# Performance work log

Hardware: AMD Instinct MI355X
Metric: run time of the kernel (lower is better)

## Reference

```python
import jax, jax.numpy as jnp
import numpy as np

N_ENT = 2000
GAT_EMB = 64
GAT_HID = 3
HIDDEN = 256
BATCH = 8
ALPHA = 0.2  # LeakyReLU negative slope
MASK_FILL = jnp.float32(9e-15)  # original fills masked-out logits with 9e-15 (NOT -inf)


def setup_inputs() -> dict:
    key = jax.random.key(0)
    k1, k2, k3, k4, k5, k6 = jax.random.split(key, 6)
    emb = jax.random.normal(k1, (N_ENT, GAT_EMB), dtype=jnp.float32)
    W = jax.random.normal(k2, (GAT_EMB, GAT_HID), dtype=jnp.float32) * 0.2
    a = jax.random.normal(k3, (2 * GAT_HID, 1), dtype=jnp.float32) * 0.2
    fc1_w = jax.random.normal(k4, (HIDDEN, N_ENT * GAT_HID), dtype=jnp.float32) * 0.02
    fc1_b = jax.random.normal(k5, (HIDDEN,), dtype=jnp.float32) * 0.02
    adj = jax.random.randint(k6, (BATCH, N_ENT, N_ENT), 0, 2, dtype=jnp.int32)
    return {"emb": emb, "W": W, "a": a, "fc1_w": fc1_w, "fc1_b": fc1_b, "adj": adj}


def reference(emb, W, a, fc1_w, fc1_b, adj):
    # h = emb @ W : [N, 3] -- shared across all graphs in the batch
    h = emb @ W
    # Pairwise logits: original concatenates [h_i, h_j] and dots with a;
    # equivalent to (h @ a1)_i + (h @ a2)_j via broadcasting (no O(N^2*2H) tensor).
    s1 = h @ a[:GAT_HID, 0]   # [N]
    s2 = h @ a[GAT_HID:, 0]   # [N]
    e = jax.nn.leaky_relu(s1[:, None] + s2[None, :], negative_slope=ALPHA)  # [N, N]
    # Mask by adjacency (fill 9e-15, matching original), softmax over neighbors (dim=1)
    masked = jnp.where(adj > 0, e[None, :, :], MASK_FILL)  # [B, N, N]
    att = jax.nn.softmax(masked, axis=2)
    # Weighted aggregation + ELU (concat=True head)
    h_prime = jnp.einsum('bij,jd->bid', att, h)  # [B, N, 3]
    x = jax.nn.elu(h_prime).reshape(att.shape[0], -1)  # [B, N*3]
    return x @ fc1_w.T + fc1_b  # [B, hidden]
```

## Files before the change

kernel.cpp:

```cpp
#include <hip/hip_runtime.h>
#include <cstddef>

#define N_ENT   2000
#define GAT_EMB 64
#define HIDDEN  256
#define BATCH   8
#define ALPHA   0.2f

typedef _Float16 half4 __attribute__((ext_vector_type(4)));
typedef int iv4 __attribute__((ext_vector_type(4)));
typedef float fv4 __attribute__((ext_vector_type(4)));

__device__ __forceinline__ iv4 nt_load4i(const int* p) {
    return __builtin_nontemporal_load((const iv4*)p);
}
__device__ __forceinline__ fv4 nt_load4f(const float* p) {
    return __builtin_nontemporal_load((const fv4*)p);
}

#define WS_HX_OFF      8192
#define WS_HY_OFF      12288
#define WS_HZ_OFF      16384
#define WS_S1_OFF      20480
#define WS_X_OFF       28672
#define WS_TABLE_BYTES 28672
#define WS_TIER2_BYTES 124672

__global__ __launch_bounds__(256) void k_init(const float* __restrict__ fc1_b,
                                              float* __restrict__ out) {
    int idx = blockIdx.x * 256 + threadIdx.x;
    out[idx] = fc1_b[idx & (HIDDEN - 1)];
}

__global__ __launch_bounds__(256) void k_prep(const float* __restrict__ emb,
                                              const float* __restrict__ W,
                                              const float* __restrict__ a,
                                              float* __restrict__ ws) {
    __shared__ float sW[GAT_EMB * 3];
    __shared__ float sa[6];
    int t = threadIdx.x;
    if (t < GAT_EMB * 3) sW[t] = W[t];
    if (t < 6)           sa[t] = a[t];
    __syncthreads();
    int i = blockIdx.x * 256 + t;
    if (i >= 2048) return;
    if (i >= N_ENT) {
        ws[i] = 0.f;
        ((_Float16*)((char*)ws + WS_HX_OFF))[i] = (_Float16)0;
        ((_Float16*)((char*)ws + WS_HY_OFF))[i] = (_Float16)0;
        ((_Float16*)((char*)ws + WS_HZ_OFF))[i] = (_Float16)0;
        ws[WS_S1_OFF / 4 + i] = 0.f;
        return;
    }
    const float4* er = (const float4*)(emb + (size_t)i * GAT_EMB);
    float h0 = 0.f, h1 = 0.f, h2 = 0.f;
#pragma unroll
    for (int k4 = 0; k4 < GAT_EMB / 4; ++k4) {
        float4 e4 = er[k4];
        int k = 4 * k4;
        h0 += e4.x * sW[(k + 0) * 3 + 0]; h1 += e4.x * sW[(k + 0) * 3 + 1]; h2 += e4.x * sW[(k + 0) * 3 + 2];
        h0 += e4.y * sW[(k + 1) * 3 + 0]; h1 += e4.y * sW[(k + 1) * 3 + 1]; h2 += e4.y * sW[(k + 1) * 3 + 2];
        h0 += e4.z * sW[(k + 2) * 3 + 0]; h1 += e4.z * sW[(k + 2) * 3 + 1]; h2 += e4.z * sW[(k + 2) * 3 + 2];
        h0 += e4.w * sW[(k + 3) * 3 + 0]; h1 += e4.w * sW[(k + 3) * 3 + 1]; h2 += e4.w * sW[(k + 3) * 3 + 2];
    }
    ws[i] = h0 * sa[3] + h1 * sa[4] + h2 * sa[5];
    ((_Float16*)((char*)ws + WS_HX_OFF))[i] = (_Float16)h0;
    ((_Float16*)((char*)ws + WS_HY_OFF))[i] = (_Float16)h1;
    ((_Float16*)((char*)ws + WS_HZ_OFF))[i] = (_Float16)h2;
    ws[WS_S1_OFF / 4 + i] = h0 * sa[0] + h1 * sa[1] + h2 * sa[2];
}

__global__ __launch_bounds__(256, 4) void k_main(const float* __restrict__ emb,
                                                 const float* __restrict__ W,
                                                 const float* __restrict__ a,
                                                 const float* __restrict__ fc1_w,
                                                 const int*   __restrict__ adj,
                                                 float* __restrict__ wsf,
                                                 int mode,
                                                 float* __restrict__ out) {
    __shared__ __align__(16) unsigned char smem[20480];
    float*    s2s = (float*)smem;
    _Float16* hxs = (_Float16*)(smem + 8192);
    _Float16* hys = (_Float16*)(smem + 12288);
    _Float16* hzs = (_Float16*)(smem + 16384);
    __shared__ float sW[GAT_EMB * 3];
    __shared__ float sa[6];
    __shared__ float s1sh[8];
    __shared__ float xblk[24];

    int t = threadIdx.x;
    int R0 = blockIdx.x * 8;
    int b  = R0 / N_ENT;
    int i_base = R0 - b * N_ENT;

    if (mode != 0) {
        const uint4* src = (const uint4*)wsf;
        uint4* dst = (uint4*)smem;
#pragma unroll
        for (int rep = 0; rep < 5; ++rep) dst[rep * 256 + t] = src[rep * 256 + t];
        if (t < 8) s1sh[t] = wsf[WS_S1_OFF / 4 + i_base + t];
    } else {
        if (t < GAT_EMB * 3) sW[t] = W[t];
        if (t < 6)           sa[t] = a[t];
        __syncthreads();
        for (int j = t; j < N_ENT; j += 256) {
            const float4* er = (const float4*)(emb + (size_t)j * GAT_EMB);
            float h0 = 0.f, h1 = 0.f, h2 = 0.f;
#pragma unroll
            for (int k4 = 0; k4 < GAT_EMB / 4; ++k4) {
                float4 e4 = er[k4];
                int k = 4 * k4;
                h0 += e4.x * sW[(k + 0) * 3 + 0]; h1 += e4.x * sW[(k + 0) * 3 + 1]; h2 += e4.x * sW[(k + 0) * 3 + 2];
                h0 += e4.y * sW[(k + 1) * 3 + 0]; h1 += e4.y * sW[(k + 1) * 3 + 1]; h2 += e4.y * sW[(k + 1) * 3 + 2];
                h0 += e4.z * sW[(k + 2) * 3 + 0]; h1 += e4.z * sW[(k + 2) * 3 + 1]; h2 += e4.z * sW[(k + 2) * 3 + 2];
                h0 += e4.w * sW[(k + 3) * 3 + 0]; h1 += e4.w * sW[(k + 3) * 3 + 1]; h2 += e4.w * sW[(k + 3) * 3 + 2];
            }
            s2s[j] = h0 * sa[3] + h1 * sa[4] + h2 * sa[5];
            hxs[j] = (_Float16)h0; hys[j] = (_Float16)h1; hzs[j] = (_Float16)h2;
            if (j >= i_base && j < i_base + 8)
                s1sh[j - i_base] = h0 * sa[0] + h1 * sa[1] + h2 * sa[2];
        }
        if (t < 2048 - N_ENT) {
            int j = N_ENT + t;
            s2s[j] = 0.f; hxs[j] = (_Float16)0; hys[j] = (_Float16)0; hzs[j] = (_Float16)0;
        }
    }
    __syncthreads();

    int lane = t & 63;
    int w    = t >> 6;
    float s1r[2];
    const int* __restrict__ rowp[2];
#pragma unroll
    for (int r = 0; r < 2; ++r) {
        s1r[r] = s1sh[2 * w + r];
        rowp[r] = adj + ((size_t)b * N_ENT + (i_base + 2 * w + r)) * N_ENT;
    }

    float acc[2][4];
#pragma unroll
    for (int r = 0; r < 2; ++r) { acc[r][0] = 0.f; acc[r][1] = 0.f; acc[r][2] = 0.f; acc[r][3] = 0.f; }

    int l4 = lane << 2;
    iv4 buf[3][2];
#pragma unroll
    for (int r = 0; r < 2; ++r) buf[0][r] = nt_load4i(rowp[r] + l4);
#pragma unroll
    for (int r = 0; r < 2; ++r) buf[1][r] = nt_load4i(rowp[r] + 256 + l4);

#pragma unroll
    for (int c = 0; c < 8; ++c) {
        if (c + 2 < 8) {
            int j2 = (c + 2) * 256 + l4;
            int jc2 = (j2 < N_ENT) ? j2 : 0;
#pragma unroll
            for (int r = 0; r < 2; ++r)
                buf[(c + 2) % 3][r] = nt_load4i(rowp[r] + jc2);
        }
        int j0 = c * 256 + l4;
        bool valid = (j0 < N_ENT);
        float vw = valid ? 1.0f : 0.0f;
        float4 s2v = *(const float4*)&s2s[j0];
        half4  hxv = *(const half4*)&hxs[j0];
        half4  hyv = *(const half4*)&hys[j0];
        half4  hzv = *(const half4*)&hzs[j0];
        float hx[4], hy[4], hz[4];
#pragma unroll
        for (int q = 0; q < 4; ++q) { hx[q] = (float)hxv[q]; hy[q] = (float)hyv[q]; hz[q] = (float)hzv[q]; }
#pragma unroll
        for (int r = 0; r < 2; ++r) {
            iv4 mv = buf[c % 3][r];
#pragma unroll
            for (int q = 0; q < 4; ++q) {
                float e  = s1r[r] + ((const float*)&s2v)[q];
                float ev = __expf(fmaxf(e, 0.f) + ALPHA * fminf(e, 0.f));
                float contrib = ((mv[q] > 0) ? ev : 1.0f) * vw;
                acc[r][0] += contrib;
                acc[r][1] += contrib * hx[q];
                acc[r][2] += contrib * hy[q];
                acc[r][3] += contrib * hz[q];
            }
        }
    }

#pragma unroll
    for (int off = 32; off > 0; off >>= 1)
#pragma unroll
        for (int r = 0; r < 2; ++r) {
            acc[r][0] += __shfl_xor(acc[r][0], off, 64);
            acc[r][1] += __shfl_xor(acc[r][1], off, 64);
            acc[r][2] += __shfl_xor(acc[r][2], off, 64);
            acc[r][3] += __shfl_xor(acc[r][3], off, 64);
        }

    if (lane == 0) {
#pragma unroll
        for (int r = 0; r < 2; ++r) {
            float inv = 1.f / acc[r][0];
            float p0 = acc[r][1] * inv, p1 = acc[r][2] * inv, p2 = acc[r][3] * inv;
            p0 = (p0 > 0.f) ? p0 : expm1f(p0);
            p1 = (p1 > 0.f) ? p1 : expm1f(p1);
            p2 = (p2 > 0.f) ? p2 : expm1f(p2);
            if (mode == 2) {
                _Float16* x16 = (_Float16*)((char*)wsf + WS_X_OFF);
                int i = i_base + 2 * w + r;
                x16[(size_t)(3 * i + 0) * 8 + b] = (_Float16)p0;
                x16[(size_t)(3 * i + 1) * 8 + b] = (_Float16)p1;
                x16[(size_t)(3 * i + 2) * 8 + b] = (_Float16)p2;
            } else {
                int cc = 3 * (2 * w + r);
                xblk[cc + 0] = p0; xblk[cc + 1] = p1; xblk[cc + 2] = p2;
            }
        }
    }

    if (mode != 2) {
        __syncthreads();
        int k = (t + R0) & 255;
        const float* wr = fc1_w + (size_t)k * (N_ENT * 3) + 3 * i_base;
        float d = 0.f;
#pragma unroll
        for (int c2 = 0; c2 < 12; ++c2) {
            float2 wv = *(const float2*)(wr + 2 * c2);
            d += xblk[2 * c2 + 0] * wv.x + xblk[2 * c2 + 1] * wv.y;
        }
        atomicAdd(&out[b * HIDDEN + k], d);
    }
}

__global__ __launch_bounds__(256) void k_fc(const _Float16* __restrict__ x16,
                                            const float* __restrict__ fc1_w,
                                            const float* __restrict__ fc1_b,
                                            float* __restrict__ out) {
    __shared__ float red[4][8];
    int t = threadIdx.x, lane = t & 63, w = t >> 6;
    int k = blockIdx.x;
    const float* __restrict__ wr = fc1_w + (size_t)k * (N_ENT * 3);
    float acc[BATCH];
#pragma unroll
    for (int b = 0; b < BATCH; ++b) acc[b] = 0.f;
#pragma unroll
    for (int it = 0; it < 6; ++it) {
        int m0 = 4 * t + 1024 * it;
        if (m0 + 3 < N_ENT * 3) {
            fv4 wv4 = nt_load4f(wr + m0);
#pragma unroll
            for (int q = 0; q < 4; ++q) {
                half4 xa = *(const half4*)(x16 + (size_t)(m0 + q) * 8);
                half4 xb = *(const half4*)(x16 + (size_t)(m0 + q) * 8 + 4);
                float wv = wv4[q];
                acc[0] += wv * (float)xa[0]; acc[1] += wv * (float)xa[1];
                acc[2] += wv * (float)xa[2]; acc[3] += wv * (float)xa[3];
                acc[4] += wv * (float)xb[0]; acc[5] += wv * (float)xb[1];
                acc[6] += wv * (float)xb[2]; acc[7] += wv * (float)xb[3];
            }
        }
    }
#pragma unroll
    for (int off = 32; off > 0; off >>= 1)
#pragma unroll
        for (int b = 0; b < BATCH; ++b) acc[b] += __shfl_xor(acc[b], off, 64);
    if (lane == 0)
#pragma unroll
        for (int b = 0; b < BATCH; ++b) red[w][b] = acc[b];
    __syncthreads();
    if (t < 8)
        out[t * HIDDEN + k] = red[0][t] + red[1][t] + red[2][t] + red[3][t] + fc1_b[k];
}

extern "C" void kernel_launch(void* const* d_in, const int* in_sizes, int n_in,
                              void* d_out, int out_size, void* d_ws, size_t ws_size,
                              hipStream_t stream) {
    const float* emb   = (const float*)d_in[0];
    const float* W     = (const float*)d_in[1];
    const float* a     = (const float*)d_in[2];
    const float* fc1_w = (const float*)d_in[3];
    const float* fc1_b = (const float*)d_in[4];
    const int*   adj   = (const int*)d_in[5];
    float* out = (float*)d_out;
    float* ws  = (float*)d_ws;
    (void)in_sizes; (void)n_in; (void)out_size;

    int tier = (ws_size >= (size_t)WS_TIER2_BYTES) ? 2
             : (ws_size >= (size_t)WS_TABLE_BYTES) ? 1 : 0;

    if (tier < 2)  k_init<<<8, 256, 0, stream>>>(fc1_b, out);
    if (tier >= 1) k_prep<<<8, 256, 0, stream>>>(emb, W, a, ws);
    k_main<<<N_ENT, 256, 0, stream>>>(emb, W, a, fc1_w, adj, ws, tier, out);
    if (tier == 2)
        k_fc<<<HIDDEN, 256, 0, stream>>>((const _Float16*)((char*)d_ws + WS_X_OFF),
                                         fc1_w, fc1_b, out);
}
```

Before: 199.7 us.

## Use 512-thread main blocks, deeper adjacency prefetch, and warp-per-row prep

The prep kernel now gives each embedding row to one wavefront, with lanes splitting the 64-wide dot product and combining it by shuffle reduction, across 512 blocks instead of 8. The main kernel moves to 1000 blocks of 512 threads covering 16 rows each, which halves the redundant per-block shared-memory table loads, and its adjacency prefetch grows from 2 to 3 chunks ahead. Register pressure rises, and the larger blocks under launch bounds of 512 may limit occupancy.

```diff
diff --git a/kernel.cpp b/kernel.cpp
--- a/kernel.cpp
+++ b/kernel.cpp
@@ -42,35 +42,28 @@
     if (t < GAT_EMB * 3) sW[t] = W[t];
     if (t < 6)           sa[t] = a[t];
     __syncthreads();
-    int i = blockIdx.x * 256 + t;
-    if (i >= 2048) return;
-    if (i >= N_ENT) {
-        ws[i] = 0.f;
-        ((_Float16*)((char*)ws + WS_HX_OFF))[i] = (_Float16)0;
-        ((_Float16*)((char*)ws + WS_HY_OFF))[i] = (_Float16)0;
-        ((_Float16*)((char*)ws + WS_HZ_OFF))[i] = (_Float16)0;
-        ws[WS_S1_OFF / 4 + i] = 0.f;
-        return;
-    }
-    const float4* er = (const float4*)(emb + (size_t)i * GAT_EMB);
-    float h0 = 0.f, h1 = 0.f, h2 = 0.f;
-#pragma unroll
-    for (int k4 = 0; k4 < GAT_EMB / 4; ++k4) {
-        float4 e4 = er[k4];
-        int k = 4 * k4;
-        h0 += e4.x * sW[(k + 0) * 3 + 0]; h1 += e4.x * sW[(k + 0) * 3 + 1]; h2 += e4.x * sW[(k + 0) * 3 + 2];
-        h0 += e4.y * sW[(k + 1) * 3 + 0]; h1 += e4.y * sW[(k + 1) * 3 + 1]; h2 += e4.y * sW[(k + 1) * 3 + 2];
-        h0 += e4.z * sW[(k + 2) * 3 + 0]; h1 += e4.z * sW[(k + 2) * 3 + 1]; h2 += e4.z * sW[(k + 2) * 3 + 2];
-        h0 += e4.w * sW[(k + 3) * 3 + 0]; h1 += e4.w * sW[(k + 3) * 3 + 1]; h2 += e4.w * sW[(k + 3) * 3 + 2];
-    }
-    ws[i] = h0 * sa[3] + h1 * sa[4] + h2 * sa[5];
-    ((_Float16*)((char*)ws + WS_HX_OFF))[i] = (_Float16)h0;
-    ((_Float16*)((char*)ws + WS_HY_OFF))[i] = (_Float16)h1;
-    ((_Float16*)((char*)ws + WS_HZ_OFF))[i] = (_Float16)h2;
-    ws[WS_S1_OFF / 4 + i] = h0 * sa[0] + h1 * sa[1] + h2 * sa[2];
-}
-
-__global__ __launch_bounds__(256, 4) void k_main(const float* __restrict__ emb,
+    int lane = t & 63, w = t >> 6;
+    int row = blockIdx.x * 4 + w;
+    float e = (row < N_ENT) ? emb[(size_t)row * GAT_EMB + lane] : 0.f;
+    float p0 = e * sW[lane * 3 + 0];
+    float p1 = e * sW[lane * 3 + 1];
+    float p2 = e * sW[lane * 3 + 2];
+#pragma unroll
+    for (int off = 32; off > 0; off >>= 1) {
+        p0 += __shfl_xor(p0, off, 64);
+        p1 += __shfl_xor(p1, off, 64);
+        p2 += __shfl_xor(p2, off, 64);
+    }
+    if (lane == 0) {
+        ws[row] = p0 * sa[3] + p1 * sa[4] + p2 * sa[5];
+        ((_Float16*)((char*)ws + WS_HX_OFF))[row] = (_Float16)p0;
+        ((_Float16*)((char*)ws + WS_HY_OFF))[row] = (_Float16)p1;
+        ((_Float16*)((char*)ws + WS_HZ_OFF))[row] = (_Float16)p2;
+        ws[WS_S1_OFF / 4 + row] = p0 * sa[0] + p1 * sa[1] + p2 * sa[2];
+    }
+}
+
+__global__ __launch_bounds__(512, 4) void k_main(const float* __restrict__ emb,
                                                  const float* __restrict__ W,
                                                  const float* __restrict__ a,
                                                  const float* __restrict__ fc1_w,
@@ -85,25 +78,27 @@
     _Float16* hzs = (_Float16*)(smem + 16384);
     __shared__ float sW[GAT_EMB * 3];
     __shared__ float sa[6];
-    __shared__ float s1sh[8];
-    __shared__ float xblk[24];
+    __shared__ float s1sh[16];
+    __shared__ float xblk[48];
 
     int t = threadIdx.x;
-    int R0 = blockIdx.x * 8;
-    int b  = R0 / N_ENT;
-    int i_base = R0 - b * N_ENT;
+    int bid = blockIdx.x;
+    int b  = bid / 125;
+    int i_base = (bid - b * 125) * 16;
+    int R0 = b * N_ENT + i_base;
 
     if (mode != 0) {
         const uint4* src = (const uint4*)wsf;
         uint4* dst = (uint4*)smem;
-#pragma unroll
-        for (int rep = 0; rep < 5; ++rep) dst[rep * 256 + t] = src[rep * 256 + t];
-        if (t < 8) s1sh[t] = wsf[WS_S1_OFF / 4 + i_base + t];
+        dst[t]        = src[t];
+        dst[512 + t]  = src[512 + t];
+        if (t < 256) dst[1024 + t] = src[1024 + t];
+        if (t < 16) s1sh[t] = wsf[WS_S1_OFF / 4 + i_base + t];
     } else {
         if (t < GAT_EMB * 3) sW[t] = W[t];
         if (t < 6)           sa[t] = a[t];
         __syncthreads();
-        for (int j = t; j < N_ENT; j += 256) {
+        for (int j = t; j < N_ENT; j += 512) {
             const float4* er = (const float4*)(emb + (size_t)j * GAT_EMB);
             float h0 = 0.f, h1 = 0.f, h2 = 0.f;
 #pragma unroll
@@ -117,7 +112,7 @@
             }
             s2s[j] = h0 * sa[3] + h1 * sa[4] + h2 * sa[5];
             hxs[j] = (_Float16)h0; hys[j] = (_Float16)h1; hzs[j] = (_Float16)h2;
-            if (j >= i_base && j < i_base + 8)
+            if (j >= i_base && j < i_base + 16)
                 s1sh[j - i_base] = h0 * sa[0] + h1 * sa[1] + h2 * sa[2];
         }
         if (t < 2048 - N_ENT) {
@@ -142,20 +137,20 @@
     for (int r = 0; r < 2; ++r) { acc[r][0] = 0.f; acc[r][1] = 0.f; acc[r][2] = 0.f; acc[r][3] = 0.f; }
 
     int l4 = lane << 2;
-    iv4 buf[3][2];
-#pragma unroll
-    for (int r = 0; r < 2; ++r) buf[0][r] = nt_load4i(rowp[r] + l4);
-#pragma unroll
-    for (int r = 0; r < 2; ++r) buf[1][r] = nt_load4i(rowp[r] + 256 + l4);
+    iv4 buf[4][2];
+#pragma unroll
+    for (int c = 0; c < 3; ++c)
+#pragma unroll
+        for (int r = 0; r < 2; ++r) buf[c][r] = nt_load4i(rowp[r] + c * 256 + l4);
 
 #pragma unroll
     for (int c = 0; c < 8; ++c) {
-        if (c + 2 < 8) {
-            int j2 = (c + 2) * 256 + l4;
+        if (c + 3 < 8) {
+            int j2 = (c + 3) * 256 + l4;
             int jc2 = (j2 < N_ENT) ? j2 : 0;
 #pragma unroll
             for (int r = 0; r < 2; ++r)
-                buf[(c + 2) % 3][r] = nt_load4i(rowp[r] + jc2);
+                buf[(c + 3) & 3][r] = nt_load4i(rowp[r] + jc2);
         }
         int j0 = c * 256 + l4;
         bool valid = (j0 < N_ENT);
@@ -169,7 +164,7 @@
         for (int q = 0; q < 4; ++q) { hx[q] = (float)hxv[q]; hy[q] = (float)hyv[q]; hz[q] = (float)hzv[q]; }
 #pragma unroll
         for (int r = 0; r < 2; ++r) {
-            iv4 mv = buf[c % 3][r];
+            iv4 mv = buf[c & 3][r];
 #pragma unroll
             for (int q = 0; q < 4; ++q) {
                 float e  = s1r[r] + ((const float*)&s2v)[q];
@@ -216,15 +211,17 @@
 
     if (mode != 2) {
         __syncthreads();
-        int k = (t + R0) & 255;
-        const float* wr = fc1_w + (size_t)k * (N_ENT * 3) + 3 * i_base;
-        float d = 0.f;
-#pragma unroll
-        for (int c2 = 0; c2 < 12; ++c2) {
-            float2 wv = *(const float2*)(wr + 2 * c2);
-            d += xblk[2 * c2 + 0] * wv.x + xblk[2 * c2 + 1] * wv.y;
-        }
-        atomicAdd(&out[b * HIDDEN + k], d);
+        if (t < 256) {
+            int k = (t + R0) & 255;
+            const float* wr = fc1_w + (size_t)k * (N_ENT * 3) + 3 * i_base;
+            float d = 0.f;
+#pragma unroll
+            for (int c2 = 0; c2 < 24; ++c2) {
+                float2 wv = *(const float2*)(wr + 2 * c2);
+                d += xblk[2 * c2 + 0] * wv.x + xblk[2 * c2 + 1] * wv.y;
+            }
+            atomicAdd(&out[b * HIDDEN + k], d);
+        }
     }
 }
 
@@ -285,8 +282,8 @@
              : (ws_size >= (size_t)WS_TABLE_BYTES) ? 1 : 0;
 
     if (tier < 2)  k_init<<<8, 256, 0, stream>>>(fc1_b, out);
-    if (tier >= 1) k_prep<<<8, 256, 0, stream>>>(emb, W, a, ws);
-    k_main<<<N_ENT, 256, 0, stream>>>(emb, W, a, fc1_w, adj, ws, tier, out);
+    if (tier >= 1) k_prep<<<512, 256, 0, stream>>>(emb, W, a, ws);
+    k_main<<<1000, 512, 0, stream>>>(emb, W, a, fc1_w, adj, ws, tier, out);
     if (tier == 2)
         k_fc<<<HIDDEN, 256, 0, stream>>>((const _Float16*)((char*)d_ws + WS_X_OFF),
                                          fc1_w, fc1_b, out);
```

Measured after the change: 195.8 us. 1.02x faster.
